# Optimization experiments

Hardware: AMD Instinct MI355X
Metric: run time of the kernel (lower is better)

The kernel has to match this reference:

```python
import jax, jax.numpy as jnp
from jax import lax
import numpy as np

K = 3
PAD = (K - 1) // 2
EPS = 1e-5


def setup_inputs() -> dict:
    key = jax.random.key(0)
    k0, k1, k2, k3 = jax.random.split(key, 4)
    B, C, O, H, W = 8, 128, 128, 64, 64
    x = jax.random.normal(k0, (B, C, H, W), jnp.float32)
    bn_gamma = jnp.ones((C,), jnp.float32)
    bn_beta = jnp.zeros((C,), jnp.float32)
    bn_mean = jnp.zeros((C,), jnp.float32)
    bn_var = jnp.ones((C,), jnp.float32)
    # small offset-conv weights -> realistic sub-pixel offsets
    w_off = jax.random.normal(k1, (2 * K * K, C, K, K), jnp.float32) * 0.01
    b_off = jnp.zeros((2 * K * K,), jnp.float32)
    w_dconv = jax.random.normal(k2, (O, C, K, K), jnp.float32) * (1.0 / np.sqrt(C * K * K))
    b_dconv = jax.random.normal(k3, (O,), jnp.float32) * 0.01
    return dict(x=x, bn_gamma=bn_gamma, bn_beta=bn_beta, bn_mean=bn_mean,
                bn_var=bn_var, w_off=w_off, b_off=b_off,
                w_dconv=w_dconv, b_dconv=b_dconv)


def _conv2d(x, w, b):
    y = lax.conv_general_dilated(
        x, w, window_strides=(1, 1), padding=[(PAD, PAD), (PAD, PAD)],
        dimension_numbers=('NCHW', 'OIHW', 'NCHW'))
    return y + b[None, :, None, None]


def _deform_conv2d(x, offsets, w, b):
    # torchvision DeformConv2d semantics (deform_groups=1, groups=1, stride=1)
    B, C, H, W = x.shape
    KK = K * K
    off = offsets.reshape(B, KK, 2, H, W)  # (dy, dx) per kernel tap
    dy, dx = off[:, :, 0], off[:, :, 1]    # [B,KK,H,W]
    kh = (jnp.arange(KK) // K).astype(x.dtype)
    kw = (jnp.arange(KK) % K).astype(x.dtype)
    # sampling positions: p0 + pk - pad + offset
    py = dy + jnp.arange(H, dtype=x.dtype)[None, None, :, None] + (kh - PAD)[None, :, None, None]
    px = dx + jnp.arange(W, dtype=x.dtype)[None, None, None, :] + (kw - PAD)[None, :, None, None]
    y0 = jnp.floor(py)
    x0 = jnp.floor(px)
    wy = py - y0
    wx = px - x0
    y0i = y0.astype(jnp.int32)
    x0i = x0.astype(jnp.int32)
    xflat = x.reshape(B, C, H * W)

    def gather(yi, xi):
        valid = (yi >= 0) & (yi < H) & (xi >= 0) & (xi < W)
        idx = jnp.clip(yi, 0, H - 1) * W + jnp.clip(xi, 0, W - 1)  # [B,KK,H,W]
        vals = jax.vmap(lambda xf, ii: xf[:, ii])(xflat, idx)      # [B,C,KK,H,W]
        return vals * valid[:, None].astype(x.dtype)

    # bilinear sample with implicit zero padding outside the image
    v = (((1 - wy) * (1 - wx))[:, None] * gather(y0i, x0i)
         + ((1 - wy) * wx)[:, None] * gather(y0i, x0i + 1)
         + (wy * (1 - wx))[:, None] * gather(y0i + 1, x0i)
         + (wy * wx)[:, None] * gather(y0i + 1, x0i + 1))  # [B,C,KK,H,W]
    out = jnp.einsum('bckhw,ock->bohw', v, w.reshape(w.shape[0], C, KK))
    return out + b[None, :, None, None]


def reference(x, bn_gamma, bn_beta, bn_mean, bn_var, w_off, b_off, w_dconv, b_dconv):
    # BN (inference form) + ReLU
    inv = bn_gamma * lax.rsqrt(bn_var + EPS)
    h = jnp.maximum((x - bn_mean[None, :, None, None]) * inv[None, :, None, None]
                    + bn_beta[None, :, None, None], 0.0)
    offsets = _conv2d(h, w_off, b_off)          # [B, 2*K*K, H, W]
    return _deform_conv2d(h, offsets, w_dconv, b_dconv)
```

## Files before the change

kernel.cpp:

```cpp
#include <hip/hip_runtime.h>

#define CC 128
#define OO 128
#define HH 64
#define WW 64
#define HW (HH*WW)

typedef __attribute__((ext_vector_type(8))) __bf16 bf16x8;
typedef __attribute__((ext_vector_type(4))) __bf16 bf16x4;
typedef __attribute__((ext_vector_type(4))) float  f32x4;

__global__ __launch_bounds__(256) void prep(
    const float* __restrict__ x,
    const float* __restrict__ gamma, const float* __restrict__ beta,
    const float* __restrict__ mean,  const float* __restrict__ var,
    const float* __restrict__ w_dconv, const float* __restrict__ w_off,
    __bf16* __restrict__ h,
    __bf16* __restrict__ wt_bf,
    __bf16* __restrict__ w_off_b)
{
    __shared__ float inv_s[128], bb_s[128];
    __shared__ __bf16 tile[64 * 130];
    int blk = blockIdx.x;
    int tid = threadIdx.x;

    if (blk >= 512) {
        int idx = (blk - 512) * 256 + tid;
        if (idx < 9 * 128 * 128) {
            int c = idx & 127, o = (idx >> 7) & 127, kk = idx >> 14;
            wt_bf[idx] = (__bf16)w_dconv[(o * 128 + c) * 9 + kk];
        }
        if (idx < 9 * 32 * 128) {
            int c = idx & 127, o = (idx >> 7) & 31, kk = idx >> 12;
            float v = (o < 18) ? w_off[o * 1152 + c * 9 + kk] : 0.f;
            w_off_b[idx] = (__bf16)v;
        }
        return;
    }

    int b = blk & 7, y = blk >> 3;
    if (tid < 128) {
        float iv = gamma[tid] * rsqrtf(var[tid] + 1e-5f);
        inv_s[tid] = iv;
        bb_s[tid]  = beta[tid] - mean[tid] * iv;
    }
    __syncthreads();

    const float* xb = x + (size_t)b * CC * HW + (size_t)y * WW;
    #pragma unroll
    for (int i = 0; i < 8; ++i) {
        int idx = i * 256 + tid;
        int c = idx >> 4, x4 = idx & 15;
        float4 v = *(const float4*)(xb + (size_t)c * HW + x4 * 4);
        float iv = inv_s[c], bb = bb_s[c];
        tile[(x4 * 4 + 0) * 130 + c] = (__bf16)fmaxf(v.x * iv + bb, 0.f);
        tile[(x4 * 4 + 1) * 130 + c] = (__bf16)fmaxf(v.y * iv + bb, 0.f);
        tile[(x4 * 4 + 2) * 130 + c] = (__bf16)fmaxf(v.z * iv + bb, 0.f);
        tile[(x4 * 4 + 3) * 130 + c] = (__bf16)fmaxf(v.w * iv + bb, 0.f);
    }
    __syncthreads();

    __bf16* hb = h + ((size_t)b * HW + (size_t)y * WW) * CC;
    #pragma unroll
    for (int i = 0; i < 2; ++i) {
        int idx = i * 256 + tid;
        int xx = idx >> 3, c16 = idx & 7;
        const uint* src = (const uint*)&tile[xx * 130 + c16 * 16];
        uint r0 = src[0], r1 = src[1], r2 = src[2], r3 = src[3];
        uint r4 = src[4], r5 = src[5], r6 = src[6], r7 = src[7];
        uint* dst = (uint*)(hb + (size_t)xx * CC + c16 * 16);
        *(uint4*)dst       = (uint4){r0, r1, r2, r3};
        *(uint4*)(dst + 4) = (uint4){r4, r5, r6, r7};
    }
}

__global__ __launch_bounds__(256) void offset_mfma(
    const __bf16* __restrict__ h,
    const __bf16* __restrict__ w_off_b,
    const float* __restrict__ b_off,
    float* __restrict__ offs)
{
    __shared__ __align__(16) __bf16 at[64 * 136];
    __shared__ __align__(16) __bf16 bt[32 * 136];
    int blk = blockIdx.x;
    int b = blk & 7, y = blk >> 3;
    int tid = threadIdx.x;
    int lane = tid & 63;
    int wv  = __builtin_amdgcn_readfirstlane(tid >> 6);
    int l15 = lane & 15, quad = lane >> 4;

    const __bf16* hb = h + (size_t)b * HW * CC;

    f32x4 acc[2];
    acc[0] = (f32x4){0.f, 0.f, 0.f, 0.f};
    acc[1] = (f32x4){0.f, 0.f, 0.f, 0.f};

    for (int kk = 0; kk < 9; ++kk) {
        int dy = kk / 3 - 1, dx = kk % 3 - 1;
        int yy = y + dy;
        bool yok = (yy >= 0) && (yy < HH);
        __syncthreads();
        #pragma unroll
        for (int i = 0; i < 4; ++i) {
            int idx = i * 256 + tid;
            int xx = idx >> 4, c8 = idx & 15;
            int xs = xx + dx;
            uint4 v = (uint4){0u, 0u, 0u, 0u};
            if (yok && xs >= 0 && xs < WW)
                v = *(const uint4*)(hb + ((size_t)yy * WW + xs) * CC + c8 * 8);
            *(uint4*)&at[xx * 136 + c8 * 8] = v;
        }
        const __bf16* wsrc = w_off_b + (size_t)kk * 32 * 128;
        #pragma unroll
        for (int i = 0; i < 2; ++i) {
            int idx = i * 256 + tid;
            int o = idx >> 4, c8 = idx & 15;
            *(uint4*)&bt[o * 136 + c8 * 8] = *(const uint4*)(wsrc + o * 128 + c8 * 8);
        }
        __syncthreads();
        #pragma unroll
        for (int ks = 0; ks < 4; ++ks) {
            int kb = ks * 32 + quad * 8;
            bf16x8 a  = *(const bf16x8*)&at[(wv * 16 + l15) * 136 + kb];
            bf16x8 b0 = *(const bf16x8*)&bt[l15 * 136 + kb];
            bf16x8 b1 = *(const bf16x8*)&bt[(16 + l15) * 136 + kb];
            acc[0] = __builtin_amdgcn_mfma_f32_16x16x32_bf16(a, b0, acc[0], 0, 0, 0);
            acc[1] = __builtin_amdgcn_mfma_f32_16x16x32_bf16(a, b1, acc[1], 0, 0, 0);
        }
    }

    size_t ob = (size_t)b * 18 * HW + (size_t)y * WW;
    #pragma unroll
    for (int nt = 0; nt < 2; ++nt) {
        int oc = nt * 16 + l15;
        if (oc < 18) {
            float bias = b_off[oc];
            #pragma unroll
            for (int r = 0; r < 4; ++r) {
                int xx = wv * 16 + quad * 4 + r;
                offs[ob + (size_t)oc * HW + xx] = acc[nt][r] + bias;
            }
        }
    }
}

__global__ __launch_bounds__(256, 2) void deform_conv_mfma(
    const __bf16* __restrict__ h,
    const float* __restrict__ offs,
    const __bf16* __restrict__ wt,
    const float* __restrict__ b_dconv,
    float* __restrict__ out)
{
    __shared__ float pw[576 * 4];
    __shared__ int   pidx[576 * 4];
    __shared__ __align__(16) __bf16 vt[64 * 136];
    __shared__ __align__(16) __bf16 wl[128 * 136];

    int blk = blockIdx.x;
    int b = blk & 7, y = blk >> 3;
    int tid = threadIdx.x;

    const __bf16* hb = h + (size_t)b * HW * CC;
    size_t offbase = (size_t)b * 18 * HW + (size_t)y * WW;

    for (int e = tid; e < 576; e += 256) {
        int kk = e >> 6, xx = e & 63;
        float dy = offs[offbase + (size_t)(2 * kk) * HW + xx];
        float dx = offs[offbase + (size_t)(2 * kk + 1) * HW + xx];
        float py = dy + (float)y + (float)(kk / 3 - 1);
        float px = dx + (float)xx + (float)(kk % 3 - 1);
        float fy = floorf(py), fx = floorf(px);
        int y0 = (int)fy, x0 = (int)fx;
        float wy = py - fy, wx = px - fx;
        int y1 = y0 + 1, x1 = x0 + 1;
        bool vy0 = (y0 >= 0) && (y0 < HH);
        bool vy1 = (y1 >= 0) && (y1 < HH);
        bool vx0 = (x0 >= 0) && (x0 < WW);
        bool vx1 = (x1 >= 0) && (x1 < WW);
        int yc0 = min(max(y0, 0), HH - 1), yc1 = min(max(y1, 0), HH - 1);
        int xc0 = min(max(x0, 0), WW - 1), xc1 = min(max(x1, 0), WW - 1);
        pw[e * 4 + 0] = (vy0 && vx0) ? (1.f - wy) * (1.f - wx) : 0.f;
        pw[e * 4 + 1] = (vy0 && vx1) ? (1.f - wy) * wx         : 0.f;
        pw[e * 4 + 2] = (vy1 && vx0) ? wy * (1.f - wx)         : 0.f;
        pw[e * 4 + 3] = (vy1 && vx1) ? wy * wx                 : 0.f;
        pidx[e * 4 + 0] = (yc0 * WW + xc0) * CC;
        pidx[e * 4 + 1] = (yc0 * WW + xc1) * CC;
        pidx[e * 4 + 2] = (yc1 * WW + xc0) * CC;
        pidx[e * 4 + 3] = (yc1 * WW + xc1) * CC;
    }

    int lane = tid & 63;
    int wv   = __builtin_amdgcn_readfirstlane(tid >> 6);
    int l15  = lane & 15, quad = lane >> 4;
    int cl   = tid & 31, xh = tid >> 5;

    f32x4 acc[4][2];
    #pragma unroll
    for (int mt = 0; mt < 4; ++mt)
        #pragma unroll
        for (int nt = 0; nt < 2; ++nt)
            acc[mt][nt] = (f32x4){0.f, 0.f, 0.f, 0.f};

    for (int kk = 0; kk < 9; ++kk) {
        __syncthreads();
        const uint4* wsrc = (const uint4*)(wt + (size_t)kk * OO * CC);
        #pragma unroll
        for (int j = 0; j < 8; ++j) {
            int idx = j * 256 + tid;
            int cs = idx & 15, o = idx >> 4;
            *(uint4*)&wl[o * 136 + cs * 8] = wsrc[idx];
        }
        #pragma unroll
        for (int j = 0; j < 8; ++j) {
            int xx = xh * 8 + j;
            int e = (kk << 6) + xx;
            float w0 = pw[e * 4 + 0], w1 = pw[e * 4 + 1];
            float w2 = pw[e * 4 + 2], w3 = pw[e * 4 + 3];
            bf16x4 t0 = *(const bf16x4*)(hb + pidx[e * 4 + 0] + cl * 4);
            bf16x4 t1 = *(const bf16x4*)(hb + pidx[e * 4 + 1] + cl * 4);
            bf16x4 t2 = *(const bf16x4*)(hb + pidx[e * 4 + 2] + cl * 4);
            bf16x4 t3 = *(const bf16x4*)(hb + pidx[e * 4 + 3] + cl * 4);
            float rx = w0 * (float)t0[0] + w1 * (float)t1[0] + w2 * (float)t2[0] + w3 * (float)t3[0];
            float ry = w0 * (float)t0[1] + w1 * (float)t1[1] + w2 * (float)t2[1] + w3 * (float)t3[1];
            float rz = w0 * (float)t0[2] + w1 * (float)t1[2] + w2 * (float)t2[2] + w3 * (float)t3[2];
            float rw = w0 * (float)t0[3] + w1 * (float)t1[3] + w2 * (float)t2[3] + w3 * (float)t3[3];
            bf16x4 pk = {(__bf16)rx, (__bf16)ry, (__bf16)rz, (__bf16)rw};
            *(bf16x4*)&vt[xx * 136 + cl * 4] = pk;
        }
        __syncthreads();
        #pragma unroll
        for (int ks = 0; ks < 4; ++ks) {
            int kb = ks * 32 + quad * 8;
            bf16x8 a0 = *(const bf16x8*)&vt[(0 * 16 + l15) * 136 + kb];
            bf16x8 a1 = *(const bf16x8*)&vt[(1 * 16 + l15) * 136 + kb];
            bf16x8 a2 = *(const bf16x8*)&vt[(2 * 16 + l15) * 136 + kb];
            bf16x8 a3 = *(const bf16x8*)&vt[(3 * 16 + l15) * 136 + kb];
            bf16x8 b0 = *(const bf16x8*)&wl[(wv * 32 + l15) * 136 + kb];
            bf16x8 b1 = *(const bf16x8*)&wl[(wv * 32 + 16 + l15) * 136 + kb];
            acc[0][0] = __builtin_amdgcn_mfma_f32_16x16x32_bf16(a0, b0, acc[0][0], 0, 0, 0);
            acc[1][0] = __builtin_amdgcn_mfma_f32_16x16x32_bf16(a1, b0, acc[1][0], 0, 0, 0);
            acc[2][0] = __builtin_amdgcn_mfma_f32_16x16x32_bf16(a2, b0, acc[2][0], 0, 0, 0);
            acc[3][0] = __builtin_amdgcn_mfma_f32_16x16x32_bf16(a3, b0, acc[3][0], 0, 0, 0);
            acc[0][1] = __builtin_amdgcn_mfma_f32_16x16x32_bf16(a0, b1, acc[0][1], 0, 0, 0);
            acc[1][1] = __builtin_amdgcn_mfma_f32_16x16x32_bf16(a1, b1, acc[1][1], 0, 0, 0);
            acc[2][1] = __builtin_amdgcn_mfma_f32_16x16x32_bf16(a2, b1, acc[2][1], 0, 0, 0);
            acc[3][1] = __builtin_amdgcn_mfma_f32_16x16x32_bf16(a3, b1, acc[3][1], 0, 0, 0);
        }
    }

    size_t ob = (size_t)b * OO * HW + (size_t)y * WW;
    #pragma unroll
    for (int nt = 0; nt < 2; ++nt) {
        int o = wv * 32 + nt * 16 + l15;
        float bias = b_dconv[o];
        #pragma unroll
        for (int mt = 0; mt < 4; ++mt) {
            int xb = mt * 16 + quad * 4;
            float4 r;
            r.x = acc[mt][nt][0] + bias;
            r.y = acc[mt][nt][1] + bias;
            r.z = acc[mt][nt][2] + bias;
            r.w = acc[mt][nt][3] + bias;
            *(float4*)&out[ob + (size_t)o * HW + xb] = r;
        }
    }
}

extern "C" void kernel_launch(void* const* d_in, const int* in_sizes, int n_in,
                              void* d_out, int out_size, void* d_ws, size_t ws_size,
                              hipStream_t stream)
{
    const float* x       = (const float*)d_in[0];
    const float* gamma   = (const float*)d_in[1];
    const float* beta    = (const float*)d_in[2];
    const float* mean    = (const float*)d_in[3];
    const float* var     = (const float*)d_in[4];
    const float* w_off   = (const float*)d_in[5];
    const float* b_off   = (const float*)d_in[6];
    const float* w_dconv = (const float*)d_in[7];
    const float* b_dconv = (const float*)d_in[8];
    float* out = (float*)d_out;

    char* ws = (char*)d_ws;
    __bf16* h_bf    = (__bf16*)ws;
    float*  offs    = (float*)(ws + 8388608);
    __bf16* wt_bf   = (__bf16*)(ws + 10747904);
    __bf16* w_off_b = (__bf16*)(ws + 11042816);

    prep<<<1232, 256, 0, stream>>>(x, gamma, beta, mean, var,
                                   w_dconv, w_off, h_bf, wt_bf, w_off_b);
    offset_mfma<<<512, 256, 0, stream>>>(h_bf, w_off_b, b_off, offs);
    deform_conv_mfma<<<512, 256, 0, stream>>>(h_bf, offs, wt_bf, b_dconv, out);
}
```

Measured before the change: 133.6 us.

## Stage three padded input rows once in offset conv, read weights from global

The offset convolution kernel now loads three padded input rows (66 columns each) into shared memory once, instead of reloading a shifted 64-row tile for each of the nine taps. The A operand for each tap is indexed directly from this staged buffer. The B weights are read straight from global memory/L2 rather than staged through LDS. This removes 17 of the 18 barriers and the repeated global loads. In exchange, LDS use per block rises to about 54KB, which may reduce occupancy, and weight reads become uncoalesced global loads inside the MFMA loop.

```diff
diff --git a/kernel.cpp b/kernel.cpp
--- a/kernel.cpp
+++ b/kernel.cpp
@@ -80,8 +80,7 @@
     const float* __restrict__ b_off,
     float* __restrict__ offs)
 {
-    __shared__ __align__(16) __bf16 at[64 * 136];
-    __shared__ __align__(16) __bf16 bt[32 * 136];
+    __shared__ __align__(16) __bf16 hrow[3 * 66 * 136];
     int blk = blockIdx.x;
     int b = blk & 7, y = blk >> 3;
     int tid = threadIdx.x;
@@ -91,39 +90,40 @@
 
     const __bf16* hb = h + (size_t)b * HW * CC;
 
+    #pragma unroll
+    for (int i = 0; i < 13; ++i) {
+        int idx = i * 256 + tid;
+        if (idx < 3168) {
+            int row = idx >> 4, c8 = idx & 15;
+            int ry = row / 66, xp = row - ry * 66;
+            int xs = xp - 1;
+            int yy = y + ry - 1;
+            uint4 v = (uint4){0u, 0u, 0u, 0u};
+            if (yy >= 0 && yy < HH && xs >= 0 && xs < WW)
+                v = *(const uint4*)(hb + ((size_t)yy * WW + xs) * CC + c8 * 8);
+            *(uint4*)&hrow[row * 136 + c8 * 8] = v;
+        }
+    }
+    __syncthreads();
+
     f32x4 acc[2];
     acc[0] = (f32x4){0.f, 0.f, 0.f, 0.f};
     acc[1] = (f32x4){0.f, 0.f, 0.f, 0.f};
 
+    int m = wv * 16 + l15;
+
+    #pragma unroll
     for (int kk = 0; kk < 9; ++kk) {
-        int dy = kk / 3 - 1, dx = kk % 3 - 1;
-        int yy = y + dy;
-        bool yok = (yy >= 0) && (yy < HH);
-        __syncthreads();
-        #pragma unroll
-        for (int i = 0; i < 4; ++i) {
-            int idx = i * 256 + tid;
-            int xx = idx >> 4, c8 = idx & 15;
-            int xs = xx + dx;
-            uint4 v = (uint4){0u, 0u, 0u, 0u};
-            if (yok && xs >= 0 && xs < WW)
-                v = *(const uint4*)(hb + ((size_t)yy * WW + xs) * CC + c8 * 8);
-            *(uint4*)&at[xx * 136 + c8 * 8] = v;
-        }
-        const __bf16* wsrc = w_off_b + (size_t)kk * 32 * 128;
-        #pragma unroll
-        for (int i = 0; i < 2; ++i) {
-            int idx = i * 256 + tid;
-            int o = idx >> 4, c8 = idx & 15;
-            *(uint4*)&bt[o * 136 + c8 * 8] = *(const uint4*)(wsrc + o * 128 + c8 * 8);
-        }
-        __syncthreads();
+        int ry  = kk / 3;
+        int dxk = kk % 3 - 1;
+        int arow = ry * 66 + m + dxk + 1;
+        const __bf16* wk = w_off_b + (size_t)kk * 32 * 128;
         #pragma unroll
         for (int ks = 0; ks < 4; ++ks) {
             int kb = ks * 32 + quad * 8;
-            bf16x8 a  = *(const bf16x8*)&at[(wv * 16 + l15) * 136 + kb];
-            bf16x8 b0 = *(const bf16x8*)&bt[l15 * 136 + kb];
-            bf16x8 b1 = *(const bf16x8*)&bt[(16 + l15) * 136 + kb];
+            bf16x8 a  = *(const bf16x8*)&hrow[arow * 136 + kb];
+            bf16x8 b0 = *(const bf16x8*)(wk + l15 * 128 + kb);
+            bf16x8 b1 = *(const bf16x8*)(wk + (16 + l15) * 128 + kb);
             acc[0] = __builtin_amdgcn_mfma_f32_16x16x32_bf16(a, b0, acc[0], 0, 0, 0);
             acc[1] = __builtin_amdgcn_mfma_f32_16x16x32_bf16(a, b1, acc[1], 0, 0, 0);
         }
```

Measured after the change: 142.8 us. 6.9% more time.

## Pre-swizzle weights into MFMA fragment order and load B directly from global

Applied to the files above, without the earlier changes.

The prep kernel now writes the deform-conv and offset-conv weights in the per-lane MFMA B-fragment order. Both MFMA kernels then load B operands straight from global memory (L2-resident) as bf16x8 instead of staging them through LDS. The activation/sampled tile becomes double-buffered, which removes one barrier per tap, and the bilinear gather now uses 8-wide bf16 loads per thread. This cuts LDS traffic and footprint (deform kernel drops the 35KB weight tile), which may raise occupancy, at the cost of per-wave global weight loads sitting on the MFMA critical path.

```diff
diff --git a/kernel.cpp b/kernel.cpp
--- a/kernel.cpp
+++ b/kernel.cpp
@@ -16,8 +16,8 @@
     const float* __restrict__ mean,  const float* __restrict__ var,
     const float* __restrict__ w_dconv, const float* __restrict__ w_off,
     __bf16* __restrict__ h,
-    __bf16* __restrict__ wt_bf,
-    __bf16* __restrict__ w_off_b)
+    __bf16* __restrict__ wt_swz,
+    __bf16* __restrict__ woff_swz)
 {
     __shared__ float inv_s[128], bb_s[128];
     __shared__ __bf16 tile[64 * 130];
@@ -26,14 +26,26 @@
 
     if (blk >= 512) {
         int idx = (blk - 512) * 256 + tid;
-        if (idx < 9 * 128 * 128) {
-            int c = idx & 127, o = (idx >> 7) & 127, kk = idx >> 14;
-            wt_bf[idx] = (__bf16)w_dconv[(o * 128 + c) * 9 + kk];
-        }
-        if (idx < 9 * 32 * 128) {
-            int c = idx & 127, o = (idx >> 7) & 31, kk = idx >> 12;
+        if (idx < 147456) {
+            int j    = idx & 7;
+            int lane = (idx >> 3) & 63;
+            int og   = (idx >> 9) & 7;
+            int ks   = (idx >> 12) & 3;
+            int kk   = idx >> 14;
+            int o = og * 16 + (lane & 15);
+            int c = ks * 32 + (lane >> 4) * 8 + j;
+            wt_swz[idx] = (__bf16)w_dconv[(o * 128 + c) * 9 + kk];
+        }
+        if (idx < 36864) {
+            int j    = idx & 7;
+            int lane = (idx >> 3) & 63;
+            int og   = (idx >> 9) & 1;
+            int ks   = (idx >> 10) & 3;
+            int kk   = idx >> 12;
+            int o = og * 16 + (lane & 15);
+            int c = ks * 32 + (lane >> 4) * 8 + j;
             float v = (o < 18) ? w_off[o * 1152 + c * 9 + kk] : 0.f;
-            w_off_b[idx] = (__bf16)v;
+            woff_swz[idx] = (__bf16)v;
         }
         return;
     }
@@ -76,12 +88,11 @@
 
 __global__ __launch_bounds__(256) void offset_mfma(
     const __bf16* __restrict__ h,
-    const __bf16* __restrict__ w_off_b,
+    const __bf16* __restrict__ woff_swz,
     const float* __restrict__ b_off,
     float* __restrict__ offs)
 {
-    __shared__ __align__(16) __bf16 at[64 * 136];
-    __shared__ __align__(16) __bf16 bt[32 * 136];
+    __shared__ __align__(16) __bf16 at[2][64 * 136];
     int blk = blockIdx.x;
     int b = blk & 7, y = blk >> 3;
     int tid = threadIdx.x;
@@ -90,16 +101,17 @@
     int l15 = lane & 15, quad = lane >> 4;
 
     const __bf16* hb = h + (size_t)b * HW * CC;
+    const bf16x8* w8 = (const bf16x8*)woff_swz;
 
     f32x4 acc[2];
     acc[0] = (f32x4){0.f, 0.f, 0.f, 0.f};
     acc[1] = (f32x4){0.f, 0.f, 0.f, 0.f};
 
     for (int kk = 0; kk < 9; ++kk) {
+        int buf = kk & 1;
         int dy = kk / 3 - 1, dx = kk % 3 - 1;
         int yy = y + dy;
         bool yok = (yy >= 0) && (yy < HH);
-        __syncthreads();
         #pragma unroll
         for (int i = 0; i < 4; ++i) {
             int idx = i * 256 + tid;
@@ -108,22 +120,15 @@
             uint4 v = (uint4){0u, 0u, 0u, 0u};
             if (yok && xs >= 0 && xs < WW)
                 v = *(const uint4*)(hb + ((size_t)yy * WW + xs) * CC + c8 * 8);
-            *(uint4*)&at[xx * 136 + c8 * 8] = v;
-        }
-        const __bf16* wsrc = w_off_b + (size_t)kk * 32 * 128;
-        #pragma unroll
-        for (int i = 0; i < 2; ++i) {
-            int idx = i * 256 + tid;
-            int o = idx >> 4, c8 = idx & 15;
-            *(uint4*)&bt[o * 136 + c8 * 8] = *(const uint4*)(wsrc + o * 128 + c8 * 8);
+            *(uint4*)&at[buf][xx * 136 + c8 * 8] = v;
         }
         __syncthreads();
         #pragma unroll
         for (int ks = 0; ks < 4; ++ks) {
             int kb = ks * 32 + quad * 8;
-            bf16x8 a  = *(const bf16x8*)&at[(wv * 16 + l15) * 136 + kb];
-            bf16x8 b0 = *(const bf16x8*)&bt[l15 * 136 + kb];
-            bf16x8 b1 = *(const bf16x8*)&bt[(16 + l15) * 136 + kb];
+            bf16x8 a  = *(const bf16x8*)&at[buf][(wv * 16 + l15) * 136 + kb];
+            bf16x8 b0 = w8[((kk * 4 + ks) * 2 + 0) * 64 + lane];
+            bf16x8 b1 = w8[((kk * 4 + ks) * 2 + 1) * 64 + lane];
             acc[0] = __builtin_amdgcn_mfma_f32_16x16x32_bf16(a, b0, acc[0], 0, 0, 0);
             acc[1] = __builtin_amdgcn_mfma_f32_16x16x32_bf16(a, b1, acc[1], 0, 0, 0);
         }
@@ -147,14 +152,13 @@
 __global__ __launch_bounds__(256, 2) void deform_conv_mfma(
     const __bf16* __restrict__ h,
     const float* __restrict__ offs,
-    const __bf16* __restrict__ wt,
+    const __bf16* __restrict__ wt_swz,
     const float* __restrict__ b_dconv,
     float* __restrict__ out)
 {
     __shared__ float pw[576 * 4];
     __shared__ int   pidx[576 * 4];
-    __shared__ __align__(16) __bf16 vt[64 * 136];
-    __shared__ __align__(16) __bf16 wl[128 * 136];
+    __shared__ __align__(16) __bf16 vt[2][64 * 136];
 
     int blk = blockIdx.x;
     int b = blk & 7, y = blk >> 3;
@@ -188,11 +192,12 @@
         pidx[e * 4 + 2] = (yc1 * WW + xc0) * CC;
         pidx[e * 4 + 3] = (yc1 * WW + xc1) * CC;
     }
+    __syncthreads();
 
     int lane = tid & 63;
     int wv   = __builtin_amdgcn_readfirstlane(tid >> 6);
     int l15  = lane & 15, quad = lane >> 4;
-    int cl   = tid & 31, xh = tid >> 5;
+    const bf16x8* w8 = (const bf16x8*)wt_swz;
 
     f32x4 acc[4][2];
     #pragma unroll
@@ -202,41 +207,37 @@
             acc[mt][nt] = (f32x4){0.f, 0.f, 0.f, 0.f};
 
     for (int kk = 0; kk < 9; ++kk) {
-        __syncthreads();
-        const uint4* wsrc = (const uint4*)(wt + (size_t)kk * OO * CC);
-        #pragma unroll
-        for (int j = 0; j < 8; ++j) {
-            int idx = j * 256 + tid;
-            int cs = idx & 15, o = idx >> 4;
-            *(uint4*)&wl[o * 136 + cs * 8] = wsrc[idx];
-        }
-        #pragma unroll
-        for (int j = 0; j < 8; ++j) {
-            int xx = xh * 8 + j;
+        int buf = kk & 1;
+        #pragma unroll
+        for (int i = 0; i < 4; ++i) {
+            int idx = i * 256 + tid;
+            int xx = idx >> 4, c8 = idx & 15;
             int e = (kk << 6) + xx;
             float w0 = pw[e * 4 + 0], w1 = pw[e * 4 + 1];
             float w2 = pw[e * 4 + 2], w3 = pw[e * 4 + 3];
-            bf16x4 t0 = *(const bf16x4*)(hb + pidx[e * 4 + 0] + cl * 4);
-            bf16x4 t1 = *(const bf16x4*)(hb + pidx[e * 4 + 1] + cl * 4);
-            bf16x4 t2 = *(const bf16x4*)(hb + pidx[e * 4 + 2] + cl * 4);
-            bf16x4 t3 = *(const bf16x4*)(hb + pidx[e * 4 + 3] + cl * 4);
-            float rx = w0 * (float)t0[0] + w1 * (float)t1[0] + w2 * (float)t2[0] + w3 * (float)t3[0];
-            float ry = w0 * (float)t0[1] + w1 * (float)t1[1] + w2 * (float)t2[1] + w3 * (float)t3[1];
-            float rz = w0 * (float)t0[2] + w1 * (float)t1[2] + w2 * (float)t2[2] + w3 * (float)t3[2];
-            float rw = w0 * (float)t0[3] + w1 * (float)t1[3] + w2 * (float)t2[3] + w3 * (float)t3[3];
-            bf16x4 pk = {(__bf16)rx, (__bf16)ry, (__bf16)rz, (__bf16)rw};
-            *(bf16x4*)&vt[xx * 136 + cl * 4] = pk;
+            bf16x8 t0 = *(const bf16x8*)(hb + pidx[e * 4 + 0] + c8 * 8);
+            bf16x8 t1 = *(const bf16x8*)(hb + pidx[e * 4 + 1] + c8 * 8);
+            bf16x8 t2 = *(const bf16x8*)(hb + pidx[e * 4 + 2] + c8 * 8);
+            bf16x8 t3 = *(const bf16x8*)(hb + pidx[e * 4 + 3] + c8 * 8);
+            bf16x8 pk;
+            #pragma unroll
+            for (int q = 0; q < 8; ++q) {
+                float v = w0 * (float)t0[q] + w1 * (float)t1[q]
+                        + w2 * (float)t2[q] + w3 * (float)t3[q];
+                pk[q] = (__bf16)v;
+            }
+            *(bf16x8*)&vt[buf][xx * 136 + c8 * 8] = pk;
         }
         __syncthreads();
         #pragma unroll
         for (int ks = 0; ks < 4; ++ks) {
             int kb = ks * 32 + quad * 8;
-            bf16x8 a0 = *(const bf16x8*)&vt[(0 * 16 + l15) * 136 + kb];
-            bf16x8 a1 = *(const bf16x8*)&vt[(1 * 16 + l15) * 136 + kb];
-            bf16x8 a2 = *(const bf16x8*)&vt[(2 * 16 + l15) * 136 + kb];
-            bf16x8 a3 = *(const bf16x8*)&vt[(3 * 16 + l15) * 136 + kb];
-            bf16x8 b0 = *(const bf16x8*)&wl[(wv * 32 + l15) * 136 + kb];
-            bf16x8 b1 = *(const bf16x8*)&wl[(wv * 32 + 16 + l15) * 136 + kb];
+            bf16x8 b0 = w8[((kk * 4 + ks) * 8 + 2 * wv + 0) * 64 + lane];
+            bf16x8 b1 = w8[((kk * 4 + ks) * 8 + 2 * wv + 1) * 64 + lane];
+            bf16x8 a0 = *(const bf16x8*)&vt[buf][(0 * 16 + l15) * 136 + kb];
+            bf16x8 a1 = *(const bf16x8*)&vt[buf][(1 * 16 + l15) * 136 + kb];
+            bf16x8 a2 = *(const bf16x8*)&vt[buf][(2 * 16 + l15) * 136 + kb];
+            bf16x8 a3 = *(const bf16x8*)&vt[buf][(3 * 16 + l15) * 136 + kb];
             acc[0][0] = __builtin_amdgcn_mfma_f32_16x16x32_bf16(a0, b0, acc[0][0], 0, 0, 0);
             acc[1][0] = __builtin_amdgcn_mfma_f32_16x16x32_bf16(a1, b0, acc[1][0], 0, 0, 0);
             acc[2][0] = __builtin_amdgcn_mfma_f32_16x16x32_bf16(a2, b0, acc[2][0], 0, 0, 0);
@@ -282,13 +283,13 @@
     float* out = (float*)d_out;
 
     char* ws = (char*)d_ws;
-    __bf16* h_bf    = (__bf16*)ws;
-    float*  offs    = (float*)(ws + 8388608);
-    __bf16* wt_bf   = (__bf16*)(ws + 10747904);
-    __bf16* w_off_b = (__bf16*)(ws + 11042816);
+    __bf16* h_bf     = (__bf16*)ws;
+    float*  offs     = (float*)(ws + 8388608);
+    __bf16* wt_swz   = (__bf16*)(ws + 10747904);
+    __bf16* woff_swz = (__bf16*)(ws + 11042816);
 
     prep<<<1232, 256, 0, stream>>>(x, gamma, beta, mean, var,
-                                   w_dconv, w_off, h_bf, wt_bf, w_off_b);
-    offset_mfma<<<512, 256, 0, stream>>>(h_bf, w_off_b, b_off, offs);
-    deform_conv_mfma<<<512, 256, 0, stream>>>(h_bf, offs, wt_bf, b_dconv, out);
-}
+                                   w_dconv, w_off, h_bf, wt_swz, woff_swz);
+    offset_mfma<<<512, 256, 0, stream>>>(h_bf, woff_swz, b_off, offs);
+    deform_conv_mfma<<<512, 256, 0, stream>>>(h_bf, offs, wt_swz, b_dconv, out);
+}
```

New measurement: 127.7 us. -4.4%, faster.
